# Optimization experiments

Measured on AMD Instinct MI355X. Metric: run time of the kernel, lower is better.

Reference implementation:

```python
import jax, jax.numpy as jnp
import numpy as np
import math

H, KV, D = 16, 8, 256
SOFT_CAP = 50.0
WINDOW = 1024
EMBED = 3584


def _rope_tables(seq_len):
    inv_freq = 1.0 / (10000.0 ** (jnp.arange(0, D, 2, dtype=jnp.float32) / D))
    pos = jnp.arange(seq_len, dtype=jnp.float32)
    freqs = jnp.outer(pos, inv_freq)            # [S, D/2]
    emb = jnp.concatenate([freqs, freqs], -1)   # [S, D]
    return jnp.cos(emb), jnp.sin(emb)


def _apply_rope(x, cos, sin):
    # x: [B, S, h, D]; cos/sin: [S, D]
    x1, x2 = jnp.split(x, 2, axis=-1)
    rot = jnp.concatenate([-x2, x1], axis=-1)
    c = cos[None, :, None, :]
    s = sin[None, :, None, :]
    return x * c + rot * s


def setup_inputs() -> dict:
    key = jax.random.key(0)
    ks = jax.random.split(key, 5)
    B, S = 2, 2048
    std = 0.02
    return {
        "hidden_states": jax.random.normal(ks[0], (B, S, EMBED), jnp.float32),
        "Wq": jax.random.normal(ks[1], (EMBED, H * D), jnp.float32) * std,
        "Wk": jax.random.normal(ks[2], (EMBED, KV * D), jnp.float32) * std,
        "Wv": jax.random.normal(ks[3], (EMBED, KV * D), jnp.float32) * std,
        "Wo": jax.random.normal(ks[4], (H * D, EMBED), jnp.float32) * std,
    }


def reference(hidden_states, Wq, Wk, Wv, Wo):
    B, S, _ = hidden_states.shape
    scale = 1.0 / math.sqrt(D)

    q = (hidden_states @ Wq).reshape(B, S, H, D)
    k = (hidden_states @ Wk).reshape(B, S, KV, D)
    v = (hidden_states @ Wv).reshape(B, S, KV, D)

    cos, sin = _rope_tables(S)
    q = _apply_rope(q, cos, sin)
    k = _apply_rope(k, cos, sin)

    # GQA: repeat kv heads to match query heads
    rep = H // KV
    k = jnp.repeat(k, rep, axis=2)  # [B, S, H, D]
    v = jnp.repeat(v, rep, axis=2)

    attn = jnp.einsum('bqhd,bkhd->bhqk', q, k) * scale
    # logit soft-cap
    attn = jnp.tanh(attn / SOFT_CAP) * SOFT_CAP
    # symmetric sliding-window mask |i-j| <= WINDOW (as in source)
    pos = jnp.arange(S)
    mask = jnp.abs(pos[:, None] - pos[None, :]) <= WINDOW  # [S, S]
    attn = jnp.where(mask[None, None, :, :], attn, -jnp.inf)

    probs = jax.nn.softmax(attn, axis=-1)
    out = jnp.einsum('bhqk,bkhd->bqhd', probs, v).reshape(B, S, H * D)
    return out @ Wo
```

## Files before the change

### kernel.cpp

```cpp
#include <hip/hip_runtime.h>
#include <stdint.h>

typedef unsigned short U16;
typedef float f32x4 __attribute__((ext_vector_type(4)));
typedef __bf16 bf16x8 __attribute__((ext_vector_type(8)));

static __device__ __forceinline__ U16 f2bf(float x) {
  union { float f; unsigned u; } v; v.f = x;
  unsigned r = v.u + 0x7FFFu + ((v.u >> 16) & 1u);
  return (U16)(r >> 16);
}
static __device__ __forceinline__ float bf2f(U16 h) {
  union { unsigned u; float f; } v; v.u = ((unsigned)h) << 16;
  return v.f;
}

static __device__ __forceinline__ void gload_lds16(const void* g, void* l) {
  __builtin_amdgcn_global_load_lds(
      (const __attribute__((address_space(1))) void*)g,
      (__attribute__((address_space(3))) void*)l, 16, 0, 0);
}

#define SBAR() __builtin_amdgcn_sched_barrier(0)

__global__ __launch_bounds__(256) void k_convert(const float* __restrict__ src,
                                                 U16* __restrict__ dst, long n) {
  long base = ((long)blockIdx.x * 256 + threadIdx.x) * 8;
  if (base >= n) return;
  const float4* s = (const float4*)(src + base);
  float4 a = s[0], b = s[1];
  U16 o[8] = { f2bf(a.x), f2bf(a.y), f2bf(a.z), f2bf(a.w),
               f2bf(b.x), f2bf(b.y), f2bf(b.z), f2bf(b.w) };
  *(uint4*)(dst + base) = *(const uint4*)o;
}

__global__ __launch_bounds__(256) void k_transpose(const float* __restrict__ src,
                                                   U16* __restrict__ dst,
                                                   int K, int N) {
  __shared__ U16 tile[32][33];
  int n0 = blockIdx.x * 32, k0 = blockIdx.y * 32;
  int tx = threadIdx.x & 31, ty = threadIdx.x >> 5;
#pragma unroll
  for (int r = 0; r < 4; ++r) {
    int k = k0 + ty + r * 8;
    tile[ty + r * 8][tx] = f2bf(src[(long)k * N + n0 + tx]);
  }
  __syncthreads();
#pragma unroll
  for (int r = 0; r < 4; ++r) {
    int n = n0 + ty + r * 8;
    dst[(long)n * K + k0 + tx] = tile[tx][ty + r * 8];
  }
}

__global__ __launch_bounds__(256) void k_vtrans(const U16* __restrict__ QKV,
                                                U16* __restrict__ VT) {
  __shared__ U16 tile[32][33];
  int s0 = blockIdx.x * 32, d0 = blockIdx.y * 32, bk = blockIdx.z;
  int b = bk >> 3, kvh = bk & 7;
  int tx = threadIdx.x & 31, ty = threadIdx.x >> 5;
  const U16* src = QKV + (long)(b * 2048) * 8192 + 6144 + kvh * 256;
#pragma unroll
  for (int r = 0; r < 4; ++r) {
    int s = s0 + ty + r * 8;
    tile[ty + r * 8][tx] = src[(long)s * 8192 + d0 + tx];
  }
  __syncthreads();
  long tbase = ((long)bk * 64 + (s0 >> 5)) * 8192;
#pragma unroll
  for (int r = 0; r < 4; ++r) {
    int d = d0 + ty + r * 8;
    VT[tbase + d * 32 + tx] = tile[tx][ty + r * 8];
  }
}

__global__ __launch_bounds__(256) void k_rope_tables(float* __restrict__ cosT,
                                                     float* __restrict__ sinT) {
  int i = blockIdx.x * 256 + threadIdx.x;
  int s = i >> 7, d = i & 127;
  float freq = expf(-9.210340371976184f * (float)d / 128.0f);
  float ang = (float)s * freq;
  cosT[i] = cosf(ang);
  sinT[i] = sinf(ang);
}

__global__ __launch_bounds__(256) void k_rope(U16* __restrict__ qkv,
                                              const float* __restrict__ cosT,
                                              const float* __restrict__ sinT) {
  int i = blockIdx.x * 256 + threadIdx.x;
  int d = i & 127;
  int hh = (i >> 7) % 24;
  int row = i / 3072;
  int s = row & 2047;
  int col = (hh < 16) ? hh * 256 + d : 4096 + (hh - 16) * 256 + d;
  long base = (long)row * 8192 + col;
  float c = cosT[s * 128 + d], sn = sinT[s * 128 + d];
  float x1 = bf2f(qkv[base]), x2 = bf2f(qkv[base + 128]);
  qkv[base]       = f2bf(x1 * c - x2 * sn);
  qkv[base + 128] = f2bf(x2 * c + x1 * sn);
}

template <int F32OUT>
__global__ __launch_bounds__(512, 1) void k_gemm8(const U16* __restrict__ A,
                                                  const U16* __restrict__ Bt,
                                                  void* __restrict__ Cv,
                                                  int M, int N, int K) {
  __shared__ __align__(16) U16 Asl[2][2][128 * 64];
  __shared__ __align__(16) U16 Bsl[2][2][128 * 64];
  int nwg = gridDim.x * gridDim.y;
  int flat = blockIdx.y * gridDim.x + blockIdx.x;
  int cpx = nwg >> 3;
  int swz = (flat & 7) * cpx + (flat >> 3);
  int bx = swz % gridDim.x, by = swz / gridDim.x;
  int t = threadIdx.x, lane = t & 63, w = t >> 6;
  int m0 = by * 256, n0 = bx * 256;
  int wm = w >> 2, wn = w & 3;
  int l15 = lane & 15, l4 = lane >> 4;
  int lofs = (l15 * 4 + l4) * 16;

  f32x4 acc[8][4] = {};
  int T = K >> 6;

  int sr = lane >> 2, sc4 = (lane & 3) * 8;
  int fA0 = (w >> 1) * 16 + sr, kA0 = (w & 1) * 32 + sc4;
  int fA1 = ((8 + w) >> 1) * 16 + sr, kA1 = ((8 + w) & 1) * 32 + sc4;
  const U16* aj0 = A + (long)(m0 + fA0) * K + kA0;
  const U16* aj1 = A + (long)(m0 + fA1) * K + kA1;
  const U16* bj0 = Bt + (long)(n0 + fA0) * K + kA0;
  const U16* bj1 = Bt + (long)(n0 + fA1) * K + kA1;

  auto stageH = [&](int op, int kt, int h) {
    int buf = kt & 1;
    int ktc = (kt < T) ? kt : 0;
    long off = (long)ktc * 64 + (long)h * 128 * K;
    if (op == 0) {
      gload_lds16(aj0 + off, (char*)&Asl[buf][h][0] + w * 1024);
      gload_lds16(aj1 + off, (char*)&Asl[buf][h][0] + 8192 + w * 1024);
    } else {
      gload_lds16(bj0 + off, (char*)&Bsl[buf][h][0] + w * 1024);
      gload_lds16(bj1 + off, (char*)&Bsl[buf][h][0] + 8192 + w * 1024);
    }
  };

  bf16x8 Ar[4][2], Bq[2][2][2];

  auto readA = [&](int buf, int r) {
    const char* base = (const char*)&Asl[buf][wm][0] + lofs;
#pragma unroll
    for (int i = 0; i < 4; ++i)
#pragma unroll
      for (int kk = 0; kk < 2; ++kk)
        Ar[i][kk] = *(const bf16x8*)(base + ((r * 4 + i) * 2 + kk) * 1024);
  };
  auto readB = [&](int buf, int c) {
    const char* base = (const char*)&Bsl[buf][wn >> 1][0] + lofs;
#pragma unroll
    for (int j = 0; j < 2; ++j)
#pragma unroll
      for (int kk = 0; kk < 2; ++kk)
        Bq[c][j][kk] = *(const bf16x8*)(base + (((wn & 1) * 4 + c * 2 + j) * 2 + kk) * 1024);
  };
  auto mfmaQ = [&](int r, int c) {
    __builtin_amdgcn_s_setprio(1);
#pragma unroll
    for (int i = 0; i < 4; ++i)
#pragma unroll
      for (int j = 0; j < 2; ++j) {
        int m = r * 4 + i, n = c * 2 + j;
        acc[m][n] = __builtin_amdgcn_mfma_f32_16x16x32_bf16(Ar[i][0], Bq[c][j][0], acc[m][n], 0, 0, 0);
        acc[m][n] = __builtin_amdgcn_mfma_f32_16x16x32_bf16(Ar[i][1], Bq[c][j][1], acc[m][n], 0, 0, 0);
      }
    __builtin_amdgcn_s_setprio(0);
  };

#define PH_SYNC() do { SBAR(); __builtin_amdgcn_s_barrier(); \
    asm volatile("s_waitcnt lgkmcnt(0)" ::: "memory"); SBAR(); } while (0)
#define PH_END() do { SBAR(); __builtin_amdgcn_s_barrier(); SBAR(); } while (0)

  stageH(0, 0, 0); stageH(0, 0, 1); stageH(1, 0, 0); stageH(1, 0, 1);
  stageH(1, 1, 0); stageH(0, 1, 0);
  asm volatile("s_waitcnt vmcnt(4)" ::: "memory");
  SBAR(); __builtin_amdgcn_s_barrier(); SBAR();

  for (int base = 0; base < T; base += 2) {
    readA(0, 0); readB(0, 0);
    stageH(0, base + 1, 1);
    PH_SYNC(); mfmaQ(0, 0); PH_END();
    readB(0, 1);
    stageH(1, base + 1, 1);
    PH_SYNC(); mfmaQ(0, 1); PH_END();
    readA(0, 1);
    stageH(1, base + 2, 0);
    PH_SYNC(); mfmaQ(1, 1); PH_END();
    stageH(0, base + 2, 0);
    PH_SYNC(); mfmaQ(1, 0);
    asm volatile("s_waitcnt vmcnt(4)" ::: "memory");
    PH_END();
    readA(1, 0); readB(1, 0);
    stageH(0, base + 2, 1);
    PH_SYNC(); mfmaQ(0, 0); PH_END();
    readB(1, 1);
    stageH(1, base + 2, 1);
    PH_SYNC(); mfmaQ(0, 1); PH_END();
    readA(1, 1);
    stageH(1, base + 3, 0);
    PH_SYNC(); mfmaQ(1, 1); PH_END();
    stageH(0, base + 3, 0);
    PH_SYNC(); mfmaQ(1, 0);
    asm volatile("s_waitcnt vmcnt(4)" ::: "memory");
    PH_END();
  }

#undef PH_SYNC
#undef PH_END

#pragma unroll
  for (int m = 0; m < 8; ++m)
#pragma unroll
    for (int jj = 0; jj < 4; ++jj) {
      int row = m0 + wm * 128 + m * 16 + l4 * 4 + jj;
      if (F32OUT) {
        float* cp = (float*)Cv + (long)row * N + n0 + wn * 64 + l15;
#pragma unroll
        for (int n = 0; n < 4; ++n) cp[n * 16] = acc[m][n][jj];
      } else {
        U16* cp = (U16*)Cv + (long)row * N + n0 + wn * 64 + l15;
#pragma unroll
        for (int n = 0; n < 4; ++n) cp[n * 16] = f2bf(acc[m][n][jj]);
      }
    }
}

__global__ __launch_bounds__(256) void k_attn(const U16* __restrict__ QKV,
                                              const U16* __restrict__ VT,
                                              U16* __restrict__ O) {
  __shared__ __align__(16) U16 Ks[2][32 * 256];
  __shared__ __align__(16) U16 Vs[2][256 * 32];
  __shared__ __align__(16) U16 Plds[4][16 * 40];
  int t = threadIdx.x, lane = t & 63, w = t >> 6;
  int flat = blockIdx.x + 32 * (blockIdx.y + 16 * blockIdx.z);
  int l = (flat & 7) * 128 + (flat >> 3);
  int qb = l & 31, h = (l >> 5) & 15, b = l >> 9;
  int s0 = qb * 64;
  int kvh = h >> 1;
  long rowOff = (long)b * 2048 * 8192;
  const U16* Qb = QKV + rowOff + h * 256;
  const U16* Kb = QKV + rowOff + 4096 + kvh * 256;
  const U16* VTb = VT + (long)(b * 8 + kvh) * 64 * 8192;

  int l15 = lane & 15, l4 = lane >> 4;

  bf16x8 qf[8];
  {
    const U16* qp = Qb + (long)(s0 + w * 16 + l15) * 8192 + l4 * 8;
#pragma unroll
    for (int kc = 0; kc < 8; ++kc) qf[kc] = *(const bf16x8*)(qp + kc * 32);
  }
  asm volatile("s_waitcnt vmcnt(0)" ::: "memory");

  f32x4 acc[16] = {};
  float mrun = -1e30f, lrun = 0.0f;
  int qpos = s0 + w * 16 + l15;

  int kstart = s0 - 1024; if (kstart < 0) kstart = 0;
  int kend = s0 + 64 + 1024; if (kend > 2048) kend = 2048;

  auto stage = [&](int buf, int k0) {
#pragma unroll
    for (int i = 0; i < 4; ++i) {
      int g = i * 256 + t;
      int row = g >> 5, c = g & 31;
      int cs = c ^ (row & 7);
      gload_lds16(Kb + (long)(k0 + row) * 8192 + cs * 8,
                  (char*)&Ks[buf][0] + i * 4096 + w * 1024);
    }
    const U16* vtile = VTb + (long)(k0 >> 5) * 8192;
#pragma unroll
    for (int i = 0; i < 4; ++i) {
      int g = i * 256 + t;
      int d = g >> 2, c = g & 3;
      int cs = c ^ ((d >> 1) & 3);
      gload_lds16(vtile + d * 32 + cs * 8,
                  (char*)&Vs[buf][0] + i * 4096 + w * 1024);
    }
  };

  auto compute = [&](int buf, int k0) {
    f32x4 sAcc[2] = {};
    __builtin_amdgcn_s_setprio(1);
#pragma unroll
    for (int kc = 0; kc < 8; ++kc) {
      int c0 = ((kc * 4 + l4) ^ (l15 & 7)) * 8;
      bf16x8 a0 = *(const bf16x8*)&Ks[buf][l15 * 256 + c0];
      bf16x8 a1 = *(const bf16x8*)&Ks[buf][(16 + l15) * 256 + c0];
      sAcc[0] = __builtin_amdgcn_mfma_f32_16x16x32_bf16(a0, qf[kc], sAcc[0], 0, 0, 0);
      sAcc[1] = __builtin_amdgcn_mfma_f32_16x16x32_bf16(a1, qf[kc], sAcc[1], 0, 0, 0);
    }
    __builtin_amdgcn_s_setprio(0);
    float sv[8];
#pragma unroll
    for (int mp = 0; mp < 2; ++mp)
#pragma unroll
      for (int jj = 0; jj < 4; ++jj) {
        int key = k0 + mp * 16 + l4 * 4 + jj;
        float x = sAcc[mp][jj] * 0.00125f;
        float ex = __expf(2.0f * x);
        float z = 50.0f * (ex - 1.0f) / (ex + 1.0f);
        int dd = qpos - key;
        if (dd < -1024 || dd > 1024) z = -3e38f;
        sv[mp * 4 + jj] = z;
      }
    float tmax = sv[0];
#pragma unroll
    for (int i = 1; i < 8; ++i) tmax = fmaxf(tmax, sv[i]);
    tmax = fmaxf(tmax, __shfl_xor(tmax, 16));
    tmax = fmaxf(tmax, __shfl_xor(tmax, 32));
    bool skipall = __all((tmax <= mrun + 8.0f) ? 1 : 0) != 0;
    float mnew = skipall ? mrun : fmaxf(mrun, tmax);
    float pex[8];
    float psum = 0.0f;
#pragma unroll
    for (int i = 0; i < 8; ++i) { pex[i] = __expf(sv[i] - mnew); psum += pex[i]; }
    psum += __shfl_xor(psum, 16);
    psum += __shfl_xor(psum, 32);
    if (skipall) {
      lrun += psum;
    } else {
      float esc = __expf(mrun - mnew);
      f32x4 ev;
#pragma unroll
      for (int jj = 0; jj < 4; ++jj) ev[jj] = __shfl(esc, l4 * 4 + jj);
#pragma unroll
      for (int n = 0; n < 16; ++n) acc[n] *= ev;
      lrun = lrun * esc + psum;
      mrun = mnew;
    }
#pragma unroll
    for (int mp = 0; mp < 2; ++mp)
#pragma unroll
      for (int j2 = 0; j2 < 2; ++j2) {
        unsigned lo = f2bf(pex[mp * 4 + j2 * 2]);
        unsigned hi = f2bf(pex[mp * 4 + j2 * 2 + 1]);
        *(unsigned*)&Plds[w][l15 * 40 + mp * 16 + l4 * 4 + j2 * 2] = lo | (hi << 16);
      }
    asm volatile("s_waitcnt lgkmcnt(0)" ::: "memory");
    __builtin_amdgcn_sched_barrier(0);
    bf16x8 pa = *(const bf16x8*)&Plds[w][l15 * 40 + l4 * 8];
    __builtin_amdgcn_s_setprio(1);
#pragma unroll
    for (int n = 0; n < 16; ++n) {
      int d = n * 16 + l15;
      int c = (l4 ^ ((d >> 1) & 3)) * 8;
      bf16x8 vb = *(const bf16x8*)&Vs[buf][d * 32 + c];
      acc[n] = __builtin_amdgcn_mfma_f32_16x16x32_bf16(pa, vb, acc[n], 0, 0, 0);
    }
    __builtin_amdgcn_s_setprio(0);
  };

  int cur = 0;
  stage(0, kstart);
  for (int k0 = kstart; k0 < kend - 32; k0 += 32) {
    stage(cur ^ 1, k0 + 32);
    asm volatile("s_waitcnt vmcnt(8)" ::: "memory");
    __builtin_amdgcn_s_barrier();
    __builtin_amdgcn_sched_barrier(0);
    compute(cur, k0);
    __builtin_amdgcn_s_barrier();
    cur ^= 1;
  }
  asm volatile("s_waitcnt vmcnt(0)" ::: "memory");
  __builtin_amdgcn_s_barrier();
  __builtin_amdgcn_sched_barrier(0);
  compute(cur, kend - 32);

  f32x4 linv;
#pragma unroll
  for (int jj = 0; jj < 4; ++jj) linv[jj] = 1.0f / __shfl(lrun, l4 * 4 + jj);
#pragma unroll
  for (int jj = 0; jj < 4; ++jj) {
    int row = s0 + w * 16 + l4 * 4 + jj;
    U16* op = O + ((long)b * 2048 + row) * 4096 + h * 256 + l15;
#pragma unroll
    for (int n = 0; n < 16; ++n) op[n * 16] = f2bf(acc[n][jj] * linv[jj]);
  }
}

extern "C" void kernel_launch(void* const* d_in, const int* in_sizes, int n_in,
                              void* d_out, int out_size, void* d_ws, size_t ws_size,
                              hipStream_t stream) {
  if (n_in < 5) return;
  const float* hid = (const float*)d_in[0];
  const float* Wq  = (const float*)d_in[1];
  const float* Wk  = (const float*)d_in[2];
  const float* Wv  = (const float*)d_in[3];
  const float* Wo  = (const float*)d_in[4];

  char* ws = (char*)d_ws;
  size_t off = 0;
  auto alloc = [&](size_t bytes) {
    char* p = ws + off;
    off += (bytes + 255) & ~(size_t)255;
    return p;
  };
  float* cosT = (float*)alloc((size_t)2048 * 128 * 4);
  float* sinT = (float*)alloc((size_t)2048 * 128 * 4);
  U16*   Xb   = (U16*)alloc((size_t)4096 * 3584 * 2);
  U16*   Wt   = (U16*)alloc((size_t)8192 * 3584 * 2);
  U16*   QKV  = (U16*)alloc((size_t)4096 * 8192 * 2);
  if (off > ws_size) return;
  U16* VT   = Xb;
  U16* Wot  = Xb;
  U16* AttO = Wt;

  k_convert<<<7168, 256, 0, stream>>>(hid, Xb, (long)4096 * 3584);
  k_transpose<<<dim3(128, 112), 256, 0, stream>>>(Wq, Wt, 3584, 4096);
  k_transpose<<<dim3(64, 112), 256, 0, stream>>>(Wk, Wt + (size_t)4096 * 3584, 3584, 2048);
  k_transpose<<<dim3(64, 112), 256, 0, stream>>>(Wv, Wt + (size_t)6144 * 3584, 3584, 2048);
  k_rope_tables<<<1024, 256, 0, stream>>>(cosT, sinT);
  k_gemm8<0><<<dim3(32, 16), 512, 0, stream>>>(Xb, Wt, QKV, 4096, 8192, 3584);
  k_vtrans<<<dim3(64, 8, 16), 256, 0, stream>>>(QKV, VT);
  k_rope<<<49152, 256, 0, stream>>>(QKV, cosT, sinT);
  k_attn<<<dim3(32, 16, 2), 256, 0, stream>>>(QKV, VT, AttO);
  k_transpose<<<dim3(112, 128), 256, 0, stream>>>(Wo, Wot, 4096, 3584);
  k_gemm8<1><<<dim3(14, 16), 512, 0, stream>>>(AttO, Wot, d_out, 4096, 3584, 4096);
}
```

Measured before the change: 700.9 us.

## Store K/V tiles in fragment-native LDS order and skip mask on interior tiles

```diff
diff --git a/kernel.cpp b/kernel.cpp
--- a/kernel.cpp
+++ b/kernel.cpp
@@ -249,6 +249,7 @@
   const U16* VTb = VT + (long)(b * 8 + kvh) * 64 * 8192;
 
   int l15 = lane & 15, l4 = lane >> 4;
+  int lofs = (l15 * 4 + l4) * 16;
 
   bf16x8 qf[8];
   {
@@ -261,38 +262,42 @@
   f32x4 acc[16] = {};
   float mrun = -1e30f, lrun = 0.0f;
   int qpos = s0 + w * 16 + l15;
+  int qlo = s0 + w * 16, qhi = qlo + 15;
 
   int kstart = s0 - 1024; if (kstart < 0) kstart = 0;
   int kend = s0 + 64 + 1024; if (kend > 2048) kend = 2048;
 
-  auto stage = [&](int buf, int k0) {
-#pragma unroll
-    for (int i = 0; i < 4; ++i) {
-      int g = i * 256 + t;
-      int row = g >> 5, c = g & 31;
-      int cs = c ^ (row & 7);
-      gload_lds16(Kb + (long)(k0 + row) * 8192 + cs * 8,
-                  (char*)&Ks[buf][0] + i * 4096 + w * 1024);
-    }
-    const U16* vtile = VTb + (long)(k0 >> 5) * 8192;
-#pragma unroll
-    for (int i = 0; i < 4; ++i) {
-      int g = i * 256 + t;
-      int d = g >> 2, c = g & 3;
-      int cs = c ^ ((d >> 1) & 3);
-      gload_lds16(vtile + d * 32 + cs * 8,
-                  (char*)&Vs[buf][0] + i * 4096 + w * 1024);
-    }
+  int sl15 = (t >> 2) & 15, sl4 = t & 3;
+  int offK[4], offV[4];
+#pragma unroll
+  for (int i = 0; i < 4; ++i) {
+    int f = i * 4 + w;
+    offK[i] = ((f >> 3) * 16 + sl15) * 8192 + (f & 7) * 32 + sl4 * 8;
+    offV[i] = (f * 16 + sl15) * 32 + sl4 * 8;
+  }
+
+  const U16* kb = Kb + (long)kstart * 8192;
+  const U16* vt0 = VTb + (long)(kstart >> 5) * 8192;
+
+  auto stage = [&](int buf) {
+#pragma unroll
+    for (int i = 0; i < 4; ++i)
+      gload_lds16(kb + offK[i], (char*)&Ks[buf][0] + i * 4096 + w * 1024);
+#pragma unroll
+    for (int i = 0; i < 4; ++i)
+      gload_lds16(vt0 + offV[i], (char*)&Vs[buf][0] + i * 4096 + w * 1024);
+    kb += (long)32 * 8192;
+    vt0 += 8192;
   };
 
   auto compute = [&](int buf, int k0) {
     f32x4 sAcc[2] = {};
+    const char* Kc = (const char*)&Ks[buf][0] + lofs;
     __builtin_amdgcn_s_setprio(1);
 #pragma unroll
     for (int kc = 0; kc < 8; ++kc) {
-      int c0 = ((kc * 4 + l4) ^ (l15 & 7)) * 8;
-      bf16x8 a0 = *(const bf16x8*)&Ks[buf][l15 * 256 + c0];
-      bf16x8 a1 = *(const bf16x8*)&Ks[buf][(16 + l15) * 256 + c0];
+      bf16x8 a0 = *(const bf16x8*)(Kc + kc * 1024);
+      bf16x8 a1 = *(const bf16x8*)(Kc + (8 + kc) * 1024);
       sAcc[0] = __builtin_amdgcn_mfma_f32_16x16x32_bf16(a0, qf[kc], sAcc[0], 0, 0, 0);
       sAcc[1] = __builtin_amdgcn_mfma_f32_16x16x32_bf16(a1, qf[kc], sAcc[1], 0, 0, 0);
     }
@@ -302,14 +307,20 @@
     for (int mp = 0; mp < 2; ++mp)
 #pragma unroll
       for (int jj = 0; jj < 4; ++jj) {
-        int key = k0 + mp * 16 + l4 * 4 + jj;
-        float x = sAcc[mp][jj] * 0.00125f;
-        float ex = __expf(2.0f * x);
-        float z = 50.0f * (ex - 1.0f) / (ex + 1.0f);
-        int dd = qpos - key;
-        if (dd < -1024 || dd > 1024) z = -3e38f;
-        sv[mp * 4 + jj] = z;
+        float ex = __expf(sAcc[mp][jj] * 0.0025f);
+        sv[mp * 4 + jj] = fmaf(-100.0f, __builtin_amdgcn_rcpf(ex + 1.0f), 50.0f);
       }
+    bool full = ((qhi - k0) <= 1024) && ((k0 + 31 - qlo) <= 1024);
+    if (!full) {
+#pragma unroll
+      for (int mp = 0; mp < 2; ++mp)
+#pragma unroll
+        for (int jj = 0; jj < 4; ++jj) {
+          int key = k0 + mp * 16 + l4 * 4 + jj;
+          int dd = qpos - key;
+          if (dd < -1024 || dd > 1024) sv[mp * 4 + jj] = -3e38f;
+        }
+    }
     float tmax = sv[0];
 #pragma unroll
     for (int i = 1; i < 8; ++i) tmax = fmaxf(tmax, sv[i]);
@@ -346,21 +357,20 @@
     asm volatile("s_waitcnt lgkmcnt(0)" ::: "memory");
     __builtin_amdgcn_sched_barrier(0);
     bf16x8 pa = *(const bf16x8*)&Plds[w][l15 * 40 + l4 * 8];
+    const char* Vc = (const char*)&Vs[buf][0] + lofs;
     __builtin_amdgcn_s_setprio(1);
 #pragma unroll
     for (int n = 0; n < 16; ++n) {
-      int d = n * 16 + l15;
-      int c = (l4 ^ ((d >> 1) & 3)) * 8;
-      bf16x8 vb = *(const bf16x8*)&Vs[buf][d * 32 + c];
+      bf16x8 vb = *(const bf16x8*)(Vc + n * 1024);
       acc[n] = __builtin_amdgcn_mfma_f32_16x16x32_bf16(pa, vb, acc[n], 0, 0, 0);
     }
     __builtin_amdgcn_s_setprio(0);
   };
 
   int cur = 0;
-  stage(0, kstart);
+  stage(0);
   for (int k0 = kstart; k0 < kend - 32; k0 += 32) {
-    stage(cur ^ 1, k0 + 32);
+    stage(cur ^ 1);
     asm volatile("s_waitcnt vmcnt(8)" ::: "memory");
     __builtin_amdgcn_s_barrier();
     __builtin_amdgcn_sched_barrier(0);
```

After: 688.8 us. Within noise of the previous version (-1.7%).
